# Optimization experiments

Hardware: AMD Instinct MI355X
Metric: run time of the kernel (lower is better)

Reference implementation:

```python
import jax, jax.numpy as jnp
import numpy as np

EMB, CLS, M_MARGIN, B = 512, 20000, 4, 256
LAMB = 1500.0 / 1.1          # AngleLoss lambda at it=1: max(5, 1500/(1+0.1*1))
LMD_INTER = 0.01
PI = 3.14159265              # constant used in original sphereface code


def setup_inputs() -> dict:
    key = jax.random.key(0)
    k1, k2, k3 = jax.random.split(key, 3)
    emb = jax.random.normal(k1, (B, EMB), dtype=jnp.float32)
    y = jax.random.randint(k2, (B,), 0, CLS)
    # weight initialized uniform(-1,1) then column-renormalized inside forward
    W = jax.random.uniform(k3, (EMB, CLS), dtype=jnp.float32, minval=-1.0, maxval=1.0)
    return {"emb": emb, "y": y, "W": W}


def _forward(emb, W, y):
    b = emb.shape[0]
    # --- ASoftmax (sphereface AngleLinear, m=4, phiflag=True) ---
    nm_W = W / jnp.linalg.norm(W, axis=0, keepdims=True)            # unit columns [E,C]
    xlen = jnp.linalg.norm(emb, axis=1, keepdims=True)              # [B,1]
    cos = jnp.clip((emb @ nm_W) / xlen, -1.0, 1.0)                  # [B,C]
    cos_m = 8.0 * cos**4 - 8.0 * cos**2 + 1.0                        # cos(4*theta)
    theta = jnp.arccos(jax.lax.stop_gradient(cos))                   # torch: acos on .data
    k = jnp.floor(M_MARGIN * theta / PI)
    sign = 1.0 - 2.0 * jnp.mod(k, 2.0)                               # (-1)^k
    phi = sign * cos_m - 2.0 * k
    cos_s = cos * xlen                                               # logits[0]
    phi_s = phi * xlen
    # --- AngleLoss (gamma=0) ---
    f = 1.0 / (1.0 + LAMB)
    onehot = jax.nn.one_hot(y, CLS, dtype=cos_s.dtype)               # [B,C]
    output = cos_s + onehot * f * (phi_s - cos_s)
    logpt = jax.nn.log_softmax(output, axis=1)
    logpt_t = jnp.take_along_axis(logpt, y[:, None], axis=1)[:, 0]
    ce = -jnp.mean(logpt_t)
    # --- MHE inter-class loss: sum_{i, j != y_i} 1/||w_{y_i} - w_j||^2 ---
    # unit columns => ||w_a - w_b||^2 = 2 - 2 <w_a, w_b>; avoids the
    # [E, B*C] scatter/repeat intermediate of the original.
    ws = nm_W[:, y]                                                  # [E,B]
    cosWW = ws.T @ nm_W                                              # [B,C]
    dist2 = jnp.maximum(2.0 - 2.0 * cosWW, 0.0)
    mask = onehot > 0.5                                              # j == y_i (z_n == 0)
    inv = jnp.where(mask, 0.0, 1.0 / jnp.where(mask, 1.0, dist2))
    inter = jnp.sum(inv) / (b * (CLS - 1))
    loss = ce + LMD_INTER * inter
    return loss, cos_s, inter


def reference(emb, y, W):
    loss, logits0, inter = _forward(emb, W, y)
    pred = jnp.argmax(logits0, axis=1)
    acc = jnp.mean((pred == y).astype(jnp.float32))
    return loss, logits0, acc, inter
```

## Files before the change

### kernel.cpp

```cpp
#include <hip/hip_runtime.h>
#include <hip/hip_bf16.h>
#include <math.h>

#define B_N   256
#define EMB_N 512
#define CLS_N 20000
#define NMB   157
#define PI_F  3.14159265f
#define F_CONST ((float)(1.1 / 1501.1))

typedef __bf16 bf16x8 __attribute__((ext_vector_type(8)));
typedef float  f32x4  __attribute__((ext_vector_type(4)));
typedef unsigned short u16x8 __attribute__((ext_vector_type(8)));

__device__ __forceinline__ unsigned short f2bf(float f) {
    unsigned u = __float_as_uint(f);
    unsigned r = (u + 0x7FFFu + ((u >> 16) & 1u)) >> 16;
    return (unsigned short)r;
}

__device__ __forceinline__ void merge4(float& M, float& S, float& VM, int& VI,
                                       float m2, float s2, float vm2, int vi2) {
    float mn = fmaxf(M, m2);
    if (mn == -INFINITY) { S = 0.f; }
    else S = S * __expf(M - mn) + s2 * __expf(m2 - mn);
    M = mn;
    if (vm2 > VM || (vm2 == VM && vi2 < VI)) { VM = vm2; VI = vi2; }
}

__global__ __launch_bounds__(256) void prep_kernel(
    const float* __restrict__ emb, const int* __restrict__ y,
    const float* __restrict__ W,
    unsigned short* __restrict__ Abf,
    float* __restrict__ xlen_a, float* __restrict__ inv_xlen_a,
    float* __restrict__ inv_wny_a, float* __restrict__ mod_val_a)
{
    const int b = blockIdx.x;
    const int t = threadIdx.x;
    const int yb = y[b];
    const float* erow = emb + (size_t)b * EMB_N;
    float se = 0.f, sw = 0.f, dt = 0.f;
    for (int e = t; e < EMB_N; e += 256) {
        float ev = erow[e];
        float wv = W[(size_t)e * CLS_N + yb];
        Abf[(size_t)b * EMB_N + e]         = f2bf(ev);
        Abf[(size_t)(B_N + b) * EMB_N + e] = f2bf(wv);
        se += ev * ev; sw += wv * wv; dt += ev * wv;
    }
    __shared__ float r0[256], r1[256], r2[256];
    r0[t] = se; r1[t] = sw; r2[t] = dt;
    __syncthreads();
    for (int s = 128; s > 0; s >>= 1) {
        if (t < s) { r0[t] += r0[t + s]; r1[t] += r1[t + s]; r2[t] += r2[t + s]; }
        __syncthreads();
    }
    if (t == 0) {
        float xlen = sqrtf(r0[0]);
        float wn   = sqrtf(r1[0]);
        float inv_x = 1.f / xlen;
        float inv_w = 1.f / wn;
        float cos_t = r2[0] * inv_w * inv_x;
        cos_t = fminf(1.f, fmaxf(-1.f, cos_t));
        float c2 = cos_t * cos_t;
        float cos_m = 8.f * c2 * c2 - 8.f * c2 + 1.f;
        float theta = acosf(cos_t);
        float k = floorf(4.f * theta / PI_F);
        float sgn = 1.f - 2.f * fmodf(k, 2.f);
        float phi = sgn * cos_m - 2.f * k;
        float cos_s = cos_t * xlen;
        float phi_s = phi * xlen;
        xlen_a[b] = xlen;
        inv_xlen_a[b] = inv_x;
        inv_wny_a[b] = inv_w;
        mod_val_a[b] = cos_s + F_CONST * (phi_s - cos_s);
    }
}

__global__ __launch_bounds__(256, 3) void mfma_gemm_kernel(
    const float* __restrict__ W, const unsigned short* __restrict__ Abf,
    const int* __restrict__ y,
    const float* __restrict__ xlen_a, const float* __restrict__ inv_xlen_a,
    const float* __restrict__ inv_wny_a,
    float* __restrict__ logits, float4* __restrict__ partials,
    float* __restrict__ inter_sum)
{
    __shared__ alignas(16) char sA[2][10240];
    __shared__ alignas(16) char sB[2][8192];
    float*  sSq   = (float*)sA;
    float*  sIwc  = (float*)((char*)sA + 2048);
    float4* sPart = (float4*)((char*)sA + 2560);
    float*  red   = (float*)((char*)sA + 6656);

    const int orig = blockIdx.x;
    const int xcd  = orig & 7;
    const int wgid = (xcd < 4 ? xcd * 79 : 316 + (xcd - 4) * 78) + (orig >> 3);
    const int tile  = wgid >> 2;
    const int slice = wgid & 3;
    const int m0    = tile * 128;
    const int gn0   = slice * 128;

    const int t    = threadIdx.x;
    const int lane = t & 63;
    const int wid  = t >> 6;
    const int wr   = wid >> 1;
    const int wc   = wid & 1;
    const int r16  = lane & 15;
    const int kh   = lane >> 4;

    const char* Bb = (const char*)Abf;

    f32x4 acc[4][4] = {};
    float2 aq[2][8];
    float ssq0 = 0.f, ssq1 = 0.f;

    const int c2 = (t & 63) * 2;
    const int ko = t >> 6;
    const int gc = min(m0 + c2, CLS_N - 2);

    #define ISSUE_A(kt, s)                                                        \
        { _Pragma("unroll")                                                       \
          for (int p = 0; p < 8; ++p)                                             \
              aq[s][p] = *reinterpret_cast<const float2*>(                        \
                  &W[(size_t)((kt) + ko * 8 + p) * CLS_N + gc]);                  \
        }

    #define ISSUE_B(kt, buf)                                                      \
        { _Pragma("unroll")                                                       \
          for (int i = 0; i < 2; ++i) {                                           \
              int slot = wid * 2 + i;                                             \
              int row  = slot * 16 + (lane >> 2);                                 \
              int srcq = (lane & 3) ^ ((lane >> 2) & 3);                          \
              __builtin_amdgcn_global_load_lds(                                   \
                  (const __attribute__((address_space(1))) unsigned int*)         \
                      (Bb + (size_t)(gn0 + row) * 1024 + (size_t)(kt) * 2         \
                          + srcq * 16),                                           \
                  (__attribute__((address_space(3))) unsigned int*)               \
                      (sB[buf] + slot * 1024),                                    \
                  16, 0, 0);                                                      \
          } }

    #define WRITE_A(s, buf)                                                       \
        { u16x8 u0, u1; float s0 = 0.f, s1 = 0.f;                                 \
          _Pragma("unroll")                                                       \
          for (int p = 0; p < 8; ++p) {                                           \
              float vx = aq[s][p].x, vy = aq[s][p].y;                             \
              u0[p] = f2bf(vx); u1[p] = f2bf(vy);                                 \
              s0 += vx * vx; s1 += vy * vy;                                       \
          }                                                                       \
          ssq0 += s0; ssq1 += s1;                                                 \
          *reinterpret_cast<u16x8*>(&sA[buf][c2 * 80 + ko * 16]) = u0;            \
          *reinterpret_cast<u16x8*>(&sA[buf][(c2 + 1) * 80 + ko * 16]) = u1; }

    #define COMPUTE(buf)                                                          \
        { bf16x8 af[4], bfr[4];                                                   \
          _Pragma("unroll")                                                       \
          for (int mi = 0; mi < 4; ++mi) {                                        \
              int row = wr * 64 + mi * 16 + r16;                                  \
              af[mi] = *reinterpret_cast<const bf16x8*>(                          \
                  &sA[buf][row * 80 + kh * 16]);                                  \
          }                                                                       \
          _Pragma("unroll")                                                       \
          for (int ni = 0; ni < 4; ++ni) {                                        \
              int rowb = wc * 64 + ni * 16 + r16;                                 \
              bfr[ni] = *reinterpret_cast<const bf16x8*>(                         \
                  &sB[buf][rowb * 64 + ((kh ^ (rowb & 3)) * 16)]);                \
          }                                                                       \
          _Pragma("unroll")                                                       \
          for (int mi = 0; mi < 4; ++mi)                                          \
              _Pragma("unroll")                                                   \
              for (int ni = 0; ni < 4; ++ni)                                      \
                  acc[mi][ni] = __builtin_amdgcn_mfma_f32_16x16x32_bf16(          \
                      af[mi], bfr[ni], acc[mi][ni], 0, 0, 0); }

    #define FENCE() __builtin_amdgcn_sched_barrier(0);

    ISSUE_A(0, 0)
    ISSUE_B(0, 0)

    #pragma unroll
    for (int tt = 0; tt < 16; ++tt) {
        if (tt < 15) {
            ISSUE_A((tt + 1) * 32, (tt + 1) & 1)
            ISSUE_B((tt + 1) * 32, (tt + 1) & 1)
            WRITE_A(tt & 1, tt & 1)
            FENCE()
            asm volatile("s_waitcnt vmcnt(10) lgkmcnt(0)" ::: "memory");
        } else {
            WRITE_A(tt & 1, tt & 1)
            FENCE()
            asm volatile("s_waitcnt vmcnt(0) lgkmcnt(0)" ::: "memory");
        }
        FENCE()
        asm volatile("s_barrier" ::: "memory");
        FENCE()
        COMPUTE(tt & 1)
        FENCE()
        asm volatile("s_barrier" ::: "memory");
        FENCE()
    }
    #undef ISSUE_A
    #undef ISSUE_B
    #undef WRITE_A
    #undef COMPUTE
    #undef FENCE

    __syncthreads();

    sSq[ko * 128 + c2]     = ssq0;
    sSq[ko * 128 + c2 + 1] = ssq1;
    __syncthreads();
    if (t < 128) {
        float s = sSq[t] + sSq[128 + t] + sSq[256 + t] + sSq[384 + t];
        sIwc[t] = rsqrtf(s);
    }
    __syncthreads();

    float iwc[4][4];
    #pragma unroll
    for (int mi = 0; mi < 4; ++mi)
        #pragma unroll
        for (int r = 0; r < 4; ++r)
            iwc[mi][r] = sIwc[wr * 64 + mi * 16 + kh * 4 + r];

    if (slice < 2) {
        #pragma unroll
        for (int ni = 0; ni < 4; ++ni) {
            int bl = wc * 64 + ni * 16 + r16;
            int b  = gn0 + bl;
            float xl  = xlen_a[b];
            float ixl = inv_xlen_a[b];
            float M = -INFINITY, S = 0.f, VM = -INFINITY; int VI = 0x7fffffff;
            #pragma unroll
            for (int mi = 0; mi < 4; ++mi) {
                int cb = m0 + wr * 64 + mi * 16 + kh * 4;
                if (cb < CLS_N) {
                    f32x4 vout;
                    #pragma unroll
                    for (int r = 0; r < 4; ++r) {
                        float cosv = acc[mi][ni][r] * iwc[mi][r] * ixl;
                        cosv = fminf(1.f, fmaxf(-1.f, cosv));
                        float v = cosv * xl;
                        vout[r] = v;
                        if (v > M) { S = S * __expf(M - v) + 1.f; M = v; }
                        else       { S += __expf(v - M); }
                        if (v > VM) { VM = v; VI = cb + r; }
                    }
                    *reinterpret_cast<f32x4*>(&logits[(size_t)b * CLS_N + cb]) = vout;
                }
            }
            #pragma unroll
            for (int d = 16; d < 64; d <<= 1) {
                float m2  = __shfl_xor(M, d);
                float s2  = __shfl_xor(S, d);
                float vm2 = __shfl_xor(VM, d);
                int   vi2 = __shfl_xor(VI, d);
                merge4(M, S, VM, VI, m2, s2, vm2, vi2);
            }
            if (kh == 0) sPart[bl * 2 + wr] = make_float4(M, S, VM, __int_as_float(VI));
        }
        __syncthreads();
        if (t < 128) {
            float4 p0 = sPart[t * 2 + 0], p1 = sPart[t * 2 + 1];
            float M = p0.x, S = p0.y, VM = p0.z; int VI = __float_as_int(p0.w);
            merge4(M, S, VM, VI, p1.x, p1.y, p1.z, __float_as_int(p1.w));
            partials[(size_t)(gn0 + t) * NMB + tile] =
                make_float4(M, S, VM, __int_as_float(VI));
        }
    } else {
        float part = 0.f;
        #pragma unroll
        for (int ni = 0; ni < 4; ++ni) {
            int b = (slice - 2) * 128 + wc * 64 + ni * 16 + r16;
            float iwy = inv_wny_a[b];
            int   yb  = y[b];
            #pragma unroll
            for (int mi = 0; mi < 4; ++mi) {
                int cb = m0 + wr * 64 + mi * 16 + kh * 4;
                #pragma unroll
                for (int r = 0; r < 4; ++r) {
                    int c = cb + r;
                    if (c < CLS_N && c != yb) {
                        float cww = acc[mi][ni][r] * iwc[mi][r] * iwy;
                        float d2 = fmaxf(2.f - 2.f * cww, 0.f);
                        part += 1.f / d2;
                    }
                }
            }
        }
        red[t] = part;
        __syncthreads();
        for (int s = 128; s > 0; s >>= 1) {
            if (t < s) red[t] += red[t + s];
            __syncthreads();
        }
        if (t == 0) atomicAdd(inter_sum, red[0]);
    }
}

__global__ __launch_bounds__(64) void reduce_kernel(
    const float4* __restrict__ partials, const float* __restrict__ logits,
    const int* __restrict__ y, const float* __restrict__ mod_val_a,
    float* __restrict__ ce_sum, float* __restrict__ acc_sum)
{
    const int b = blockIdx.x;
    const int t = threadIdx.x;
    float M = -INFINITY, S = 0.f, VM = -INFINITY; int VI = 0x7fffffff;
    for (int i = t; i < NMB; i += 64) {
        float4 p = partials[(size_t)b * NMB + i];
        merge4(M, S, VM, VI, p.x, p.y, p.z, __float_as_int(p.w));
    }
    #pragma unroll
    for (int d = 1; d < 64; d <<= 1) {
        float m2  = __shfl_xor(M, d);
        float s2  = __shfl_xor(S, d);
        float vm2 = __shfl_xor(VM, d);
        int   vi2 = __shfl_xor(VI, d);
        merge4(M, S, VM, VI, m2, s2, vm2, vi2);
    }
    if (t == 0) {
        int   yb  = y[b];
        float vyb = logits[(size_t)b * CLS_N + yb];
        float mv  = mod_val_a[b];
        float m2 = fmaxf(M, mv);
        float s2 = S * __expf(M - m2) - __expf(vyb - m2) + __expf(mv - m2);
        float lse = m2 + logf(s2);
        atomicAdd(ce_sum, -(mv - lse));
        if (VI == yb) atomicAdd(acc_sum, 1.f);
    }
}

__global__ void finalize_kernel(const float* __restrict__ accums, float* __restrict__ out)
{
    float ce    = accums[0] / (float)B_N;
    float acc   = accums[1] / (float)B_N;
    float inter = accums[2] / (float)((double)B_N * (CLS_N - 1));
    out[0] = ce + 0.01f * inter;
    out[(size_t)1 + (size_t)B_N * CLS_N + 0] = acc;
    out[(size_t)1 + (size_t)B_N * CLS_N + 1] = inter;
}

extern "C" void kernel_launch(void* const* d_in, const int* in_sizes, int n_in,
                              void* d_out, int out_size, void* d_ws, size_t ws_size,
                              hipStream_t stream) {
    const float* emb = (const float*)d_in[0];
    const int*   y   = (const int*)d_in[1];
    const float* W   = (const float*)d_in[2];
    float* out = (float*)d_out;
    float* logits = out + 1;

    const size_t ABF_OFF  = 0;
    const size_t PART_OFF = 524288;
    const size_t SC_OFF   = PART_OFF + (size_t)B_N * NMB * 16;

    unsigned short* Abf = (unsigned short*)((char*)d_ws + ABF_OFF);
    float4* partials   = (float4*)((char*)d_ws + PART_OFF);
    float*  xlen_a     = (float*)((char*)d_ws + SC_OFF);
    float*  inv_xlen_a = xlen_a + 256;
    float*  inv_wny_a  = xlen_a + 512;
    float*  mod_val_a  = xlen_a + 768;
    float*  accums     = xlen_a + 1024;

    hipMemsetAsync(accums, 0, 3 * sizeof(float), stream);

    prep_kernel<<<B_N, 256, 0, stream>>>(emb, y, W, Abf,
                                         xlen_a, inv_xlen_a, inv_wny_a, mod_val_a);
    mfma_gemm_kernel<<<628, 256, 0, stream>>>(W, Abf, y,
                                              xlen_a, inv_xlen_a, inv_wny_a,
                                              logits, partials, accums + 2);
    reduce_kernel<<<B_N, 64, 0, stream>>>(partials, logits, y, mod_val_a,
                                          accums + 0, accums + 1);
    finalize_kernel<<<1, 1, 0, stream>>>(accums, out);
}
```

Measured before the change: 55.93 us.

## Pre-convert W to transposed bf16 and stream both GEMM operands via direct LDS loads

The prep kernel gains 628 extra blocks that transpose W into a padded, class-major bf16 buffer and accumulate per-class squared norms with atomics. The GEMM then loads both operands with global_load_lds instead of loading fp32 W into registers, converting it and writing it to LDS. This removes the register staging and conversion work from the main loop and lets occupancy rise to 4 blocks. The cost is an extra full pass over W (read fp32, write bf16), an extra memset, and roughly 20 MB more workspace traffic.

```diff
diff --git a/kernel.cpp b/kernel.cpp
--- a/kernel.cpp
+++ b/kernel.cpp
@@ -5,13 +5,13 @@
 #define B_N   256
 #define EMB_N 512
 #define CLS_N 20000
+#define CLS_PAD 20096
 #define NMB   157
 #define PI_F  3.14159265f
 #define F_CONST ((float)(1.1 / 1501.1))
 
 typedef __bf16 bf16x8 __attribute__((ext_vector_type(8)));
 typedef float  f32x4  __attribute__((ext_vector_type(4)));
-typedef unsigned short u16x8 __attribute__((ext_vector_type(8)));
 
 __device__ __forceinline__ unsigned short f2bf(float f) {
     unsigned u = __float_as_uint(f);
@@ -28,68 +28,112 @@
     if (vm2 > VM || (vm2 == VM && vi2 < VI)) { VM = vm2; VI = vi2; }
 }
 
-__global__ __launch_bounds__(256) void prep_kernel(
+__global__ __launch_bounds__(256) void prep_convert_kernel(
     const float* __restrict__ emb, const int* __restrict__ y,
     const float* __restrict__ W,
-    unsigned short* __restrict__ Abf,
+    unsigned short* __restrict__ Abf, unsigned short* __restrict__ Wt,
+    float* __restrict__ colsumsq,
     float* __restrict__ xlen_a, float* __restrict__ inv_xlen_a,
     float* __restrict__ inv_wny_a, float* __restrict__ mod_val_a)
 {
-    const int b = blockIdx.x;
+    __shared__ alignas(16) char uLDS[128 * 136 * 2];
     const int t = threadIdx.x;
-    const int yb = y[b];
-    const float* erow = emb + (size_t)b * EMB_N;
-    float se = 0.f, sw = 0.f, dt = 0.f;
-    for (int e = t; e < EMB_N; e += 256) {
-        float ev = erow[e];
-        float wv = W[(size_t)e * CLS_N + yb];
-        Abf[(size_t)b * EMB_N + e]         = f2bf(ev);
-        Abf[(size_t)(B_N + b) * EMB_N + e] = f2bf(wv);
-        se += ev * ev; sw += wv * wv; dt += ev * wv;
-    }
-    __shared__ float r0[256], r1[256], r2[256];
-    r0[t] = se; r1[t] = sw; r2[t] = dt;
-    __syncthreads();
-    for (int s = 128; s > 0; s >>= 1) {
-        if (t < s) { r0[t] += r0[t + s]; r1[t] += r1[t + s]; r2[t] += r2[t + s]; }
+
+    if (blockIdx.x < 628) {
+        unsigned short (*T)[136] = (unsigned short (*)[136])uLDS;
+        const int cb = blockIdx.x;
+        const int c0 = (cb >> 2) * 128;
+        const int k0 = (cb & 3) * 128;
+        const int cl = (t & 31) * 4;
+        const int kr = t >> 5;
+        float ssq[4] = {0.f, 0.f, 0.f, 0.f};
+
+        for (int it = 0; it < 16; ++it) {
+            int k = k0 + it * 8 + kr;
+            int c = c0 + cl;
+            float4 v;
+            if (c + 3 < CLS_N) {
+                v = *reinterpret_cast<const float4*>(&W[(size_t)k * CLS_N + c]);
+            } else {
+                v.x = (c + 0 < CLS_N) ? W[(size_t)k * CLS_N + c + 0] : 0.f;
+                v.y = (c + 1 < CLS_N) ? W[(size_t)k * CLS_N + c + 1] : 0.f;
+                v.z = (c + 2 < CLS_N) ? W[(size_t)k * CLS_N + c + 2] : 0.f;
+                v.w = (c + 3 < CLS_N) ? W[(size_t)k * CLS_N + c + 3] : 0.f;
+            }
+            float vv[4] = {v.x, v.y, v.z, v.w};
+            #pragma unroll
+            for (int j = 0; j < 4; ++j) {
+                ssq[j] += vv[j] * vv[j];
+                T[cl + j][it * 8 + kr] = f2bf(vv[j]);
+            }
+        }
+        #pragma unroll
+        for (int j = 0; j < 4; ++j) {
+            int c = c0 + cl + j;
+            if (c < CLS_N) atomicAdd(&colsumsq[c], ssq[j]);
+        }
         __syncthreads();
-    }
-    if (t == 0) {
-        float xlen = sqrtf(r0[0]);
-        float wn   = sqrtf(r1[0]);
-        float inv_x = 1.f / xlen;
-        float inv_w = 1.f / wn;
-        float cos_t = r2[0] * inv_w * inv_x;
-        cos_t = fminf(1.f, fmaxf(-1.f, cos_t));
-        float c2 = cos_t * cos_t;
-        float cos_m = 8.f * c2 * c2 - 8.f * c2 + 1.f;
-        float theta = acosf(cos_t);
-        float k = floorf(4.f * theta / PI_F);
-        float sgn = 1.f - 2.f * fmodf(k, 2.f);
-        float phi = sgn * cos_m - 2.f * k;
-        float cos_s = cos_t * xlen;
-        float phi_s = phi * xlen;
-        xlen_a[b] = xlen;
-        inv_xlen_a[b] = inv_x;
-        inv_wny_a[b] = inv_w;
-        mod_val_a[b] = cos_s + F_CONST * (phi_s - cos_s);
-    }
-}
-
-__global__ __launch_bounds__(256, 3) void mfma_gemm_kernel(
-    const float* __restrict__ W, const unsigned short* __restrict__ Abf,
-    const int* __restrict__ y,
+        for (int p = 0; p < 8; ++p) {
+            int c = p * 16 + (t >> 4);
+            uint4 d = *reinterpret_cast<const uint4*>(&T[c][(t & 15) * 8]);
+            *reinterpret_cast<uint4*>(&Wt[(size_t)(c0 + c) * EMB_N + k0 + (t & 15) * 8]) = d;
+        }
+    } else {
+        float* r0 = (float*)uLDS;
+        float* r1 = r0 + 256;
+        float* r2 = r0 + 512;
+        const int b = blockIdx.x - 628;
+        const int yb = y[b];
+        const float* erow = emb + (size_t)b * EMB_N;
+        float se = 0.f, sw = 0.f, dt = 0.f;
+        for (int e = t; e < EMB_N; e += 256) {
+            float ev = erow[e];
+            float wv = W[(size_t)e * CLS_N + yb];
+            Abf[(size_t)b * EMB_N + e]         = f2bf(ev);
+            Abf[(size_t)(B_N + b) * EMB_N + e] = f2bf(wv);
+            se += ev * ev; sw += wv * wv; dt += ev * wv;
+        }
+        r0[t] = se; r1[t] = sw; r2[t] = dt;
+        __syncthreads();
+        for (int s = 128; s > 0; s >>= 1) {
+            if (t < s) { r0[t] += r0[t + s]; r1[t] += r1[t + s]; r2[t] += r2[t + s]; }
+            __syncthreads();
+        }
+        if (t == 0) {
+            float xlen = sqrtf(r0[0]);
+            float wn   = sqrtf(r1[0]);
+            float inv_x = 1.f / xlen;
+            float inv_w = 1.f / wn;
+            float cos_t = r2[0] * inv_w * inv_x;
+            cos_t = fminf(1.f, fmaxf(-1.f, cos_t));
+            float c2 = cos_t * cos_t;
+            float cos_m = 8.f * c2 * c2 - 8.f * c2 + 1.f;
+            float theta = acosf(cos_t);
+            float k = floorf(4.f * theta / PI_F);
+            float sgn = 1.f - 2.f * fmodf(k, 2.f);
+            float phi = sgn * cos_m - 2.f * k;
+            float cos_s = cos_t * xlen;
+            float phi_s = phi * xlen;
+            xlen_a[b] = xlen;
+            inv_xlen_a[b] = inv_x;
+            inv_wny_a[b] = inv_w;
+            mod_val_a[b] = cos_s + F_CONST * (phi_s - cos_s);
+        }
+    }
+}
+
+__global__ __launch_bounds__(256, 4) void mfma_gemm_kernel(
+    const unsigned short* __restrict__ Wt, const unsigned short* __restrict__ Abf,
+    const float* __restrict__ colsumsq, const int* __restrict__ y,
     const float* __restrict__ xlen_a, const float* __restrict__ inv_xlen_a,
     const float* __restrict__ inv_wny_a,
     float* __restrict__ logits, float4* __restrict__ partials,
     float* __restrict__ inter_sum)
 {
-    __shared__ alignas(16) char sA[2][10240];
-    __shared__ alignas(16) char sB[2][8192];
-    float*  sSq   = (float*)sA;
-    float*  sIwc  = (float*)((char*)sA + 2048);
-    float4* sPart = (float4*)((char*)sA + 2560);
-    float*  red   = (float*)((char*)sA + 6656);
+    __shared__ alignas(16) char smem[32768];
+    float*  sIwc  = (float*)smem;
+    float4* sPart = (float4*)(smem + 512);
+    float*  red   = (float*)(smem + 4608);
 
     const int orig = blockIdx.x;
     const int xcd  = orig & 7;
@@ -107,63 +151,42 @@
     const int r16  = lane & 15;
     const int kh   = lane >> 4;
 
+    const char* Ab = (const char*)Wt;
     const char* Bb = (const char*)Abf;
 
     f32x4 acc[4][4] = {};
-    float2 aq[2][8];
-    float ssq0 = 0.f, ssq1 = 0.f;
-
-    const int c2 = (t & 63) * 2;
-    const int ko = t >> 6;
-    const int gc = min(m0 + c2, CLS_N - 2);
-
-    #define ISSUE_A(kt, s)                                                        \
-        { _Pragma("unroll")                                                       \
-          for (int p = 0; p < 8; ++p)                                             \
-              aq[s][p] = *reinterpret_cast<const float2*>(                        \
-                  &W[(size_t)((kt) + ko * 8 + p) * CLS_N + gc]);                  \
-        }
-
-    #define ISSUE_B(kt, buf)                                                      \
+
+    const int srow = lane >> 2;
+    const int srcq = (lane & 3) ^ ((lane >> 2) & 3);
+
+    #define ISSUE_TILE(srcb, row0, kt, dstoff)                                    \
         { _Pragma("unroll")                                                       \
           for (int i = 0; i < 2; ++i) {                                           \
               int slot = wid * 2 + i;                                             \
-              int row  = slot * 16 + (lane >> 2);                                 \
-              int srcq = (lane & 3) ^ ((lane >> 2) & 3);                          \
+              int row  = slot * 16 + srow;                                        \
               __builtin_amdgcn_global_load_lds(                                   \
                   (const __attribute__((address_space(1))) unsigned int*)         \
-                      (Bb + (size_t)(gn0 + row) * 1024 + (size_t)(kt) * 2         \
-                          + srcq * 16),                                           \
+                      ((srcb) + (size_t)((row0) + row) * 1024                     \
+                          + (size_t)(kt) * 2 + srcq * 16),                        \
                   (__attribute__((address_space(3))) unsigned int*)               \
-                      (sB[buf] + slot * 1024),                                    \
+                      (smem + (dstoff) + slot * 1024),                            \
                   16, 0, 0);                                                      \
           } }
 
-    #define WRITE_A(s, buf)                                                       \
-        { u16x8 u0, u1; float s0 = 0.f, s1 = 0.f;                                 \
-          _Pragma("unroll")                                                       \
-          for (int p = 0; p < 8; ++p) {                                           \
-              float vx = aq[s][p].x, vy = aq[s][p].y;                             \
-              u0[p] = f2bf(vx); u1[p] = f2bf(vy);                                 \
-              s0 += vx * vx; s1 += vy * vy;                                       \
-          }                                                                       \
-          ssq0 += s0; ssq1 += s1;                                                 \
-          *reinterpret_cast<u16x8*>(&sA[buf][c2 * 80 + ko * 16]) = u0;            \
-          *reinterpret_cast<u16x8*>(&sA[buf][(c2 + 1) * 80 + ko * 16]) = u1; }
-
-    #define COMPUTE(buf)                                                          \
+    #define COMPUTE(bi)                                                           \
         { bf16x8 af[4], bfr[4];                                                   \
           _Pragma("unroll")                                                       \
           for (int mi = 0; mi < 4; ++mi) {                                        \
               int row = wr * 64 + mi * 16 + r16;                                  \
               af[mi] = *reinterpret_cast<const bf16x8*>(                          \
-                  &sA[buf][row * 80 + kh * 16]);                                  \
+                  smem + (bi) * 8192 + row * 64 + ((kh ^ (row & 3)) << 4));       \
           }                                                                       \
           _Pragma("unroll")                                                       \
           for (int ni = 0; ni < 4; ++ni) {                                        \
               int rowb = wc * 64 + ni * 16 + r16;                                 \
               bfr[ni] = *reinterpret_cast<const bf16x8*>(                         \
-                  &sB[buf][rowb * 64 + ((kh ^ (rowb & 3)) * 16)]);                \
+                  smem + 16384 + (bi) * 8192 + rowb * 64                          \
+                  + ((kh ^ (rowb & 3)) << 4));                                    \
           }                                                                       \
           _Pragma("unroll")                                                       \
           for (int mi = 0; mi < 4; ++mi)                                          \
@@ -174,21 +197,19 @@
 
     #define FENCE() __builtin_amdgcn_sched_barrier(0);
 
-    ISSUE_A(0, 0)
-    ISSUE_B(0, 0)
+    ISSUE_TILE(Ab, m0, 0, 0)
+    ISSUE_TILE(Bb, gn0, 0, 16384)
 
     #pragma unroll
     for (int tt = 0; tt < 16; ++tt) {
         if (tt < 15) {
-            ISSUE_A((tt + 1) * 32, (tt + 1) & 1)
-            ISSUE_B((tt + 1) * 32, (tt + 1) & 1)
-            WRITE_A(tt & 1, tt & 1)
+            ISSUE_TILE(Ab, m0, (tt + 1) * 32, ((tt + 1) & 1) * 8192)
+            ISSUE_TILE(Bb, gn0, (tt + 1) * 32, 16384 + ((tt + 1) & 1) * 8192)
             FENCE()
-            asm volatile("s_waitcnt vmcnt(10) lgkmcnt(0)" ::: "memory");
+            asm volatile("s_waitcnt vmcnt(4)" ::: "memory");
         } else {
-            WRITE_A(tt & 1, tt & 1)
             FENCE()
-            asm volatile("s_waitcnt vmcnt(0) lgkmcnt(0)" ::: "memory");
+            asm volatile("s_waitcnt vmcnt(0)" ::: "memory");
         }
         FENCE()
         asm volatile("s_barrier" ::: "memory");
@@ -198,20 +219,15 @@
         asm volatile("s_barrier" ::: "memory");
         FENCE()
     }
-    #undef ISSUE_A
-    #undef ISSUE_B
-    #undef WRITE_A
+    #undef ISSUE_TILE
     #undef COMPUTE
     #undef FENCE
 
     __syncthreads();
 
-    sSq[ko * 128 + c2]     = ssq0;
-    sSq[ko * 128 + c2 + 1] = ssq1;
-    __syncthreads();
     if (t < 128) {
-        float s = sSq[t] + sSq[128 + t] + sSq[256 + t] + sSq[384 + t];
-        sIwc[t] = rsqrtf(s);
+        int c = m0 + t;
+        sIwc[t] = rsqrtf(c < CLS_N ? colsumsq[c] : 1.f);
     }
     __syncthreads();
 
@@ -349,10 +365,14 @@
     float* logits = out + 1;
 
     const size_t ABF_OFF  = 0;
-    const size_t PART_OFF = 524288;
+    const size_t WT_OFF   = 524288;
+    const size_t CS_OFF   = WT_OFF + (size_t)CLS_PAD * EMB_N * 2;
+    const size_t PART_OFF = CS_OFF + (size_t)CLS_PAD * 4;
     const size_t SC_OFF   = PART_OFF + (size_t)B_N * NMB * 16;
 
     unsigned short* Abf = (unsigned short*)((char*)d_ws + ABF_OFF);
+    unsigned short* Wt  = (unsigned short*)((char*)d_ws + WT_OFF);
+    float*  colsumsq   = (float*)((char*)d_ws + CS_OFF);
     float4* partials   = (float4*)((char*)d_ws + PART_OFF);
     float*  xlen_a     = (float*)((char*)d_ws + SC_OFF);
     float*  inv_xlen_a = xlen_a + 256;
@@ -360,11 +380,12 @@
     float*  mod_val_a  = xlen_a + 768;
     float*  accums     = xlen_a + 1024;
 
+    hipMemsetAsync(colsumsq, 0, (size_t)CLS_PAD * 4, stream);
     hipMemsetAsync(accums, 0, 3 * sizeof(float), stream);
 
-    prep_kernel<<<B_N, 256, 0, stream>>>(emb, y, W, Abf,
-                                         xlen_a, inv_xlen_a, inv_wny_a, mod_val_a);
-    mfma_gemm_kernel<<<628, 256, 0, stream>>>(W, Abf, y,
+    prep_convert_kernel<<<884, 256, 0, stream>>>(emb, y, W, Abf, Wt, colsumsq,
+                                                 xlen_a, inv_xlen_a, inv_wny_a, mod_val_a);
+    mfma_gemm_kernel<<<628, 256, 0, stream>>>(Wt, Abf, colsumsq, y,
                                               xlen_a, inv_xlen_a, inv_wny_a,
                                               logits, partials, accums + 2);
     reduce_kernel<<<B_N, 64, 0, stream>>>(partials, logits, y, mod_val_a,
```

New measurement: 71.77 us. 1.28x slower.

## Deepen GEMM prefetch pipeline to two tiles ahead with four B slabs

Applied to the files above, without the earlier changes.

The GEMM main loop now keeps global loads two k-tiles ahead instead of one. W register prefetch moves to a two-slot ring, and B LDS staging moves to a four-slab ring in a single unified shared buffer. Waitcnt thresholds are adjusted to match. This aims to hide more global memory latency, at the cost of more LDS (about 52KB per block) and more live registers, which may lower occupancy below the launch bound target.

```diff
diff --git a/kernel.cpp b/kernel.cpp
--- a/kernel.cpp
+++ b/kernel.cpp
@@ -84,12 +84,11 @@
     float* __restrict__ logits, float4* __restrict__ partials,
     float* __restrict__ inter_sum)
 {
-    __shared__ alignas(16) char sA[2][10240];
-    __shared__ alignas(16) char sB[2][8192];
-    float*  sSq   = (float*)sA;
-    float*  sIwc  = (float*)((char*)sA + 2048);
-    float4* sPart = (float4*)((char*)sA + 2560);
-    float*  red   = (float*)((char*)sA + 6656);
+    __shared__ alignas(16) char smem[53248];
+    float*  sSq   = (float*)smem;
+    float*  sIwc  = (float*)(smem + 2048);
+    float4* sPart = (float4*)(smem + 2560);
+    float*  red   = (float*)(smem + 6656);
 
     const int orig = blockIdx.x;
     const int xcd  = orig & 7;
@@ -117,6 +116,9 @@
     const int ko = t >> 6;
     const int gc = min(m0 + c2, CLS_N - 2);
 
+    const int srow = lane >> 2;
+    const int srcq = (lane & 3) ^ ((lane >> 2) & 3);
+
     #define ISSUE_A(kt, s)                                                        \
         { _Pragma("unroll")                                                       \
           for (int p = 0; p < 8; ++p)                                             \
@@ -124,18 +126,17 @@
                   &W[(size_t)((kt) + ko * 8 + p) * CLS_N + gc]);                  \
         }
 
-    #define ISSUE_B(kt, buf)                                                      \
+    #define ISSUE_B(kt, slab)                                                     \
         { _Pragma("unroll")                                                       \
           for (int i = 0; i < 2; ++i) {                                           \
               int slot = wid * 2 + i;                                             \
-              int row  = slot * 16 + (lane >> 2);                                 \
-              int srcq = (lane & 3) ^ ((lane >> 2) & 3);                          \
+              int row  = slot * 16 + srow;                                        \
               __builtin_amdgcn_global_load_lds(                                   \
                   (const __attribute__((address_space(1))) unsigned int*)         \
                       (Bb + (size_t)(gn0 + row) * 1024 + (size_t)(kt) * 2         \
                           + srcq * 16),                                           \
                   (__attribute__((address_space(3))) unsigned int*)               \
-                      (sB[buf] + slot * 1024),                                    \
+                      (smem + 20480 + (slab) * 8192 + slot * 1024),               \
                   16, 0, 0);                                                      \
           } }
 
@@ -148,22 +149,23 @@
               s0 += vx * vx; s1 += vy * vy;                                       \
           }                                                                       \
           ssq0 += s0; ssq1 += s1;                                                 \
-          *reinterpret_cast<u16x8*>(&sA[buf][c2 * 80 + ko * 16]) = u0;            \
-          *reinterpret_cast<u16x8*>(&sA[buf][(c2 + 1) * 80 + ko * 16]) = u1; }
-
-    #define COMPUTE(buf)                                                          \
+          *reinterpret_cast<u16x8*>(smem + (buf) * 10240 + c2 * 80 + ko * 16) = u0; \
+          *reinterpret_cast<u16x8*>(smem + (buf) * 10240 + (c2 + 1) * 80 + ko * 16) = u1; }
+
+    #define COMPUTE(buf, slab)                                                    \
         { bf16x8 af[4], bfr[4];                                                   \
           _Pragma("unroll")                                                       \
           for (int mi = 0; mi < 4; ++mi) {                                        \
               int row = wr * 64 + mi * 16 + r16;                                  \
               af[mi] = *reinterpret_cast<const bf16x8*>(                          \
-                  &sA[buf][row * 80 + kh * 16]);                                  \
+                  smem + (buf) * 10240 + row * 80 + kh * 16);                     \
           }                                                                       \
           _Pragma("unroll")                                                       \
           for (int ni = 0; ni < 4; ++ni) {                                        \
               int rowb = wc * 64 + ni * 16 + r16;                                 \
               bfr[ni] = *reinterpret_cast<const bf16x8*>(                         \
-                  &sB[buf][rowb * 64 + ((kh ^ (rowb & 3)) * 16)]);                \
+                  smem + 20480 + (slab) * 8192 + rowb * 64                        \
+                  + ((kh ^ (rowb & 3)) << 4));                                    \
           }                                                                       \
           _Pragma("unroll")                                                       \
           for (int mi = 0; mi < 4; ++mi)                                          \
@@ -174,26 +176,28 @@
 
     #define FENCE() __builtin_amdgcn_sched_barrier(0);
 
-    ISSUE_A(0, 0)
-    ISSUE_B(0, 0)
+    ISSUE_A(0, 0)  ISSUE_B(0, 0)
+    ISSUE_A(32, 1) ISSUE_B(32, 1)
 
     #pragma unroll
     for (int tt = 0; tt < 16; ++tt) {
-        if (tt < 15) {
-            ISSUE_A((tt + 1) * 32, (tt + 1) & 1)
-            ISSUE_B((tt + 1) * 32, (tt + 1) & 1)
-            WRITE_A(tt & 1, tt & 1)
+        WRITE_A(tt & 1, tt & 1)
+        if (tt <= 13) {
+            ISSUE_A((tt + 2) * 32, tt & 1)
+            ISSUE_B((tt + 2) * 32, (tt + 2) & 3)
+            FENCE()
+            asm volatile("s_waitcnt vmcnt(20) lgkmcnt(0)" ::: "memory");
+        } else if (tt == 14) {
             FENCE()
             asm volatile("s_waitcnt vmcnt(10) lgkmcnt(0)" ::: "memory");
         } else {
-            WRITE_A(tt & 1, tt & 1)
             FENCE()
             asm volatile("s_waitcnt vmcnt(0) lgkmcnt(0)" ::: "memory");
         }
         FENCE()
         asm volatile("s_barrier" ::: "memory");
         FENCE()
-        COMPUTE(tt & 1)
+        COMPUTE(tt & 1, tt & 3)
         FENCE()
         asm volatile("s_barrier" ::: "memory");
         FENCE()
```

New measurement: 59.52 us. +6.4%, slower.
